# Kernel optimization log

Hardware: AMD Instinct MI355X
Metric: run time of the kernel (lower is better)

The kernel has to match this reference:

```python
import jax, jax.numpy as jnp
import numpy as np

B = 8; N_MELS = 128; T_LEN = 1024; PH = 16; PW = 16
D = 768          # embed_dim
DEPTH = 12
N = 16           # d_state
K = 4            # d_conv (mamba default)
E = 2 * D        # d_inner (expand=2)
R = 48           # dt_rank = ceil(D/16)
NC = 10
LP = (N_MELS // PH) * (T_LEN // PW)   # 512 patch tokens
MID = LP // 2                          # middle cls token position


def layer_norm(x, w, b, eps=1e-5):
    m = x.mean(-1, keepdims=True)
    v = ((x - m) ** 2).mean(-1, keepdims=True)
    return (x - m) * jax.lax.rsqrt(v + eps) * w + b


def dw_conv(x, w, b):
    # x: (B,L,E), w: (E,K) -> causal depthwise conv1d + SiLU (mamba conv branch)
    xt = jnp.transpose(x, (0, 2, 1))
    y = jax.lax.conv_general_dilated(xt, w[:, None, :], (1,), [(K - 1, 0)],
                                     feature_group_count=E,
                                     dimension_numbers=('NCH', 'OIH', 'NCH'))
    return jax.nn.silu(jnp.transpose(y + b[None, :, None], (0, 2, 1)))


def ssm(u, z, xw, dtw, dtb, A_log, Dp):
    # selective scan: u,z (B,L,E); xw (R+2N,E); dtw (E,R); A_log,Dp (E,N)/(E,)
    dbc = jnp.einsum('ble,re->blr', u, xw)
    dt, Bm, Cm = dbc[..., :R], dbc[..., R:R + N], dbc[..., R + N:]
    delta = jax.nn.softplus(jnp.einsum('blr,er->ble', dt, dtw) + dtb)
    A = -jnp.exp(A_log)  # (E,N)

    def step(h, inp):
        d_t, B_t, C_t, u_t = inp  # (B,E),(B,N),(B,N),(B,E)
        h = h * jnp.exp(d_t[:, :, None] * A) + (d_t * u_t)[:, :, None] * B_t[:, None, :]
        return h, jnp.einsum('ben,bn->be', h, C_t)

    h0 = jnp.zeros((u.shape[0], E, N), u.dtype)
    xs = (jnp.transpose(delta, (1, 0, 2)), jnp.transpose(Bm, (1, 0, 2)),
          jnp.transpose(Cm, (1, 0, 2)), jnp.transpose(u, (1, 0, 2)))
    _, ys = jax.lax.scan(step, h0, xs)
    y = jnp.transpose(ys, (1, 0, 2)) + u * Dp
    return y * jax.nn.silu(z)


def setup_inputs() -> dict:
    key = jax.random.key(0)
    kit = iter(jax.random.split(key, 64))
    def nrm(shape, s=0.02):
        return jax.random.normal(next(kit), shape, jnp.float32) * s
    inp = {}
    inp['x'] = jax.random.normal(next(kit), (B, 1, N_MELS, T_LEN), jnp.float32)
    inp['patch_w'] = nrm((D, 1, PH, PW))
    inp['patch_b'] = jnp.zeros((D,), jnp.float32)
    inp['cls_token'] = nrm((1, 1, D))
    inp['norm_w'] = jnp.ones((DEPTH, D), jnp.float32)
    inp['norm_b'] = jnp.zeros((DEPTH, D), jnp.float32)
    inp['in_proj_w'] = nrm((DEPTH, 2 * E, D))
    for s in ('f', 'b'):
        inp['conv_w_' + s] = nrm((DEPTH, E, K), 0.1)
        inp['conv_b_' + s] = jnp.zeros((DEPTH, E), jnp.float32)
        inp['x_proj_w_' + s] = nrm((DEPTH, R + 2 * N, E))
        inp['dt_proj_w_' + s] = nrm((DEPTH, E, R), 0.1)
        dt = jnp.exp(jax.random.uniform(next(kit), (DEPTH, E), jnp.float32)
                     * (np.log(0.1) - np.log(1e-3)) + np.log(1e-3))
        inp['dt_proj_b_' + s] = jnp.log(jnp.expm1(dt))  # inverse softplus init
        inp['A_log_' + s] = jnp.broadcast_to(
            jnp.log(jnp.arange(1, N + 1, dtype=jnp.float32)), (DEPTH, E, N)) + jnp.zeros((DEPTH, E, N), jnp.float32)
        inp['D_' + s] = jnp.ones((DEPTH, E), jnp.float32)
    inp['out_proj_w'] = nrm((DEPTH, D, E))
    inp['fnorm_w'] = jnp.ones((D,), jnp.float32)
    inp['fnorm_b'] = jnp.zeros((D,), jnp.float32)
    inp['head_norm_w'] = jnp.ones((D,), jnp.float32)
    inp['head_norm_b'] = jnp.zeros((D,), jnp.float32)
    inp['head_w'] = nrm((NC, D))
    inp['head_b'] = jnp.zeros((NC,), jnp.float32)
    return inp


def reference(x, patch_w, patch_b, cls_token, norm_w, norm_b, in_proj_w,
              conv_w_f, conv_b_f, conv_w_b, conv_b_b,
              x_proj_w_f, x_proj_w_b, dt_proj_w_f, dt_proj_b_f,
              dt_proj_w_b, dt_proj_b_b, A_log_f, A_log_b, D_f, D_b,
              out_proj_w, fnorm_w, fnorm_b, head_norm_w, head_norm_b,
              head_w, head_b):
    # patch embed (Conv2d, stride = patch)
    t = jax.lax.conv_general_dilated(x, patch_w, (PH, PW), 'VALID',
                                     dimension_numbers=('NCHW', 'OIHW', 'NCHW'))
    t = t + patch_b[None, :, None, None]
    b = t.shape[0]
    tok = jnp.transpose(t.reshape(b, D, -1), (0, 2, 1))  # (B, LP, D)
    cls = jnp.broadcast_to(cls_token, (b, 1, D))
    h = jnp.concatenate([tok[:, :MID], cls, tok[:, MID:]], axis=1)  # middle cls token
    for i in range(DEPTH):
        hn = layer_norm(h, norm_w[i], norm_b[i])
        xz = jnp.einsum('bld,ed->ble', hn, in_proj_w[i])
        xm, z = xz[..., :E], xz[..., E:]
        # forward direction
        xf = dw_conv(xm, conv_w_f[i], conv_b_f[i])
        yf = ssm(xf, z, x_proj_w_f[i], dt_proj_w_f[i], dt_proj_b_f[i], A_log_f[i], D_f[i])
        # backward direction (bimamba v2): scan over flipped sequence
        xr, zr = xm[:, ::-1], z[:, ::-1]
        xb = dw_conv(xr, conv_w_b[i], conv_b_b[i])
        yb = ssm(xb, zr, x_proj_w_b[i], dt_proj_w_b[i], dt_proj_b_b[i], A_log_b[i], D_b[i])[:, ::-1]
        h = h + jnp.einsum('ble,de->bld', yf + yb, out_proj_w[i])
    h = layer_norm(h, fnorm_w, fnorm_b)
    feat = h[:, MID]  # middle cls token feature
    feat = layer_norm(feat, head_norm_w, head_norm_b)
    return jnp.einsum('bd,cd->bc', feat, head_w) + head_b
```

## Files before the change

### kernel.cpp

```cpp
#include <hip/hip_runtime.h>
#include <cstddef>
#include <cstdint>

#define NB     8
#define L_SEQ  513
#define DMODEL 768
#define EDIM   1536
#define XZDIM  3072
#define NSTATE 16
#define DBCW   80
#define RDIM   48
#define ROWS   (NB*L_SEQ)
#define RE     ((size_t)ROWS*EDIM)
#define KSPLIT_DBC 8

typedef unsigned short u16;
typedef __bf16 bf16x8 __attribute__((ext_vector_type(8)));
typedef float  f32x4  __attribute__((ext_vector_type(4)));

__device__ __forceinline__ u16 f2b(float f) {
  uint32_t x = __float_as_uint(f);
  uint32_t r = x + 0x7fffu + ((x >> 16) & 1u);
  return (u16)(r >> 16);
}
__device__ __forceinline__ float b2flo(uint32_t w){ return __uint_as_float(w << 16); }
__device__ __forceinline__ float b2fhi(uint32_t w){ return __uint_as_float(w & 0xffff0000u); }

__device__ __forceinline__ void glds16(const void* g, void* l) {
  __builtin_amdgcn_global_load_lds(
      (const __attribute__((address_space(1))) uint32_t*)g,
      (__attribute__((address_space(3))) uint32_t*)l, 16, 0, 0);
}

__global__ __launch_bounds__(256) void f2b_k(const float* __restrict__ in,
                                             u16* __restrict__ out, int n)
{
  int i = (blockIdx.x*256 + threadIdx.x) * 4;
  if (i >= n) return;
  float4 v = *reinterpret_cast<const float4*>(in + i);
  ushort4 o;
  o.x = f2b(v.x); o.y = f2b(v.y); o.z = f2b(v.z); o.w = f2b(v.w);
  *reinterpret_cast<ushort4*>(out + i) = o;
}

__global__ __launch_bounds__(256) void f2b2_k(const float* __restrict__ a,
                                              const float* __restrict__ b,
                                              u16* __restrict__ oa,
                                              u16* __restrict__ ob,
                                              int n1, int n2)
{
  int i = (blockIdx.x*256 + threadIdx.x) * 4;
  if (i < n1) {
    float4 v = *reinterpret_cast<const float4*>(a + i);
    ushort4 o; o.x=f2b(v.x); o.y=f2b(v.y); o.z=f2b(v.z); o.w=f2b(v.w);
    *reinterpret_cast<ushort4*>(oa + i) = o;
  } else {
    int j = i - n1;
    if (j < n2) {
      float4 v = *reinterpret_cast<const float4*>(b + j);
      ushort4 o; o.x=f2b(v.x); o.y=f2b(v.y); o.z=f2b(v.z); o.w=f2b(v.w);
      int row = j / EDIM, col = j - row*EDIM;
      u16* dst = ob + (size_t)row*XZDIM + col;
      *reinterpret_cast<ushort4*>(dst)        = o;
      *reinterpret_cast<ushort4*>(dst + EDIM) = o;
    }
  }
}

__global__ __launch_bounds__(256) void cvt_dtw_k(const float* __restrict__ in,
                                                 u16* __restrict__ out, int nrows)
{
  int idx = blockIdx.x*256 + threadIdx.x;
  if (idx >= nrows*16) return;
  int row = idx >> 4, c4 = (idx & 15) * 4;
  ushort4 o; o.x = o.y = o.z = o.w = 0;
  if (c4 < RDIM) {
    float4 v = *reinterpret_cast<const float4*>(in + (size_t)row*RDIM + c4);
    o.x = f2b(v.x); o.y = f2b(v.y); o.z = f2b(v.z); o.w = f2b(v.w);
  }
  *reinterpret_cast<ushort4*>(out + (size_t)row*64 + c4) = o;
}

__global__ __launch_bounds__(256) void im2col_k(const float* __restrict__ x,
                                                u16* __restrict__ P)
{
  int idx = blockIdx.x*256 + threadIdx.x;
  int col4 = (idx & 63) * 4;
  int r = idx >> 6;
  int b = r >> 9, p = r & 511;
  int ph = p >> 6, pcol = p & 63;
  int i = col4 >> 4, j = col4 & 15;
  const float* src = x + (size_t)b*131072 + (size_t)(ph*16 + i)*1024 + pcol*16 + j;
  float4 v = *reinterpret_cast<const float4*>(src);
  ushort4 o;
  o.x = f2b(v.x); o.y = f2b(v.y); o.z = f2b(v.z); o.w = f2b(v.w);
  *reinterpret_cast<ushort4*>(P + (size_t)r*256 + col4) = o;
}

__global__ __launch_bounds__(256) void insert_k(const float* __restrict__ tokf,
                                                const float* __restrict__ cls,
                                                float* __restrict__ h)
{
  int idx = blockIdx.x*256 + threadIdx.x;
  if (idx >= ROWS*192) return;
  int d4 = (idx % 192) * 4;
  int row = idx / 192;
  int b = row / L_SEQ, l = row - b*L_SEQ;
  float4 v;
  if (l == 256) v = *reinterpret_cast<const float4*>(cls + d4);
  else {
    int p = (l < 256) ? l : l - 1;
    v = *reinterpret_cast<const float4*>(tokf + ((size_t)(b*512 + p))*DMODEL + d4);
  }
  *reinterpret_cast<float4*>(h + (size_t)row*DMODEL + d4) = v;
}

__device__ __forceinline__ void wave_reduce2(float& s, float& ss) {
  #pragma unroll
  for (int o = 32; o; o >>= 1) { s += __shfl_down(s, o); ss += __shfl_down(ss, o); }
}

__global__ __launch_bounds__(256) void layernorm_k(
    const float* __restrict__ x, const float* __restrict__ w,
    const float* __restrict__ b, u16* __restrict__ y)
{
  int row = blockIdx.x;
  const float* xr = x + (size_t)row*DMODEL;
  u16*         yr = y + (size_t)row*DMODEL;
  int t = threadIdx.x;
  float v0 = xr[t], v1 = xr[t+256], v2 = xr[t+512];
  float s = v0+v1+v2, ss = v0*v0 + v1*v1 + v2*v2;
  wave_reduce2(s, ss);
  __shared__ float sm[8];
  if ((t & 63) == 0) { sm[t>>6] = s; sm[4 + (t>>6)] = ss; }
  __syncthreads();
  s  = sm[0]+sm[1]+sm[2]+sm[3];
  ss = sm[4]+sm[5]+sm[6]+sm[7];
  float mean = s * (1.f/768.f);
  float var  = ss * (1.f/768.f) - mean*mean;
  float rstd = rsqrtf(var + 1e-5f);
  yr[t]     = f2b((v0-mean)*rstd*w[t]     + b[t]);
  yr[t+256] = f2b((v1-mean)*rstd*w[t+256] + b[t+256]);
  yr[t+512] = f2b((v2-mean)*rstd*w[t+512] + b[t+512]);
}

__global__ __launch_bounds__(256) void gemm_bf16_k(
    const u16* __restrict__ A, int lda,
    const u16* __restrict__ W, int ldw,
    float* __restrict__ C, u16* __restrict__ Cb,
    int ldc, int M, int Ncols, int K,
    const float* __restrict__ bias, int epilogue,
    int zsplit, size_t bsA, size_t bsW, size_t bsC, size_t bsBias)
{
  __shared__ __align__(16) u16 Asl[2][4096];
  __shared__ __align__(16) u16 Wsl[2][4096];
  const int tid = threadIdx.x;
  const int bm = blockIdx.y << 7, bn = blockIdx.x << 7;
  const int wv = tid >> 6, ln = tid & 63;
  const int wr = (wv >> 1) << 6, wc = (wv & 1) << 6;

  int kb = 0, ke = K;
  {
    int zb = (int)blockIdx.z;
    int dir = zb / zsplit, kslab = zb - dir*zsplit;
    A += (size_t)dir * bsA;
    W += (size_t)dir * bsW;
    if (C)  C  += (size_t)dir * bsC;
    if (Cb) Cb += (size_t)dir * bsC;
    if (bias) bias += (size_t)dir * bsBias;
    if (zsplit > 1) {
      int ksl = K / zsplit;
      kb = kslab * ksl; ke = kb + ksl;
      C += (size_t)kslab * (size_t)M * (size_t)ldc;
    }
  }

  const int q0 = (ln >> 4) * 8;
  const int r0 = wv*16 + (ln & 15);
  const int r1 = (wv+4)*16 + (ln & 15);

  int ar0 = bm + r0; if (ar0 >= M) ar0 = M-1;
  int ar1 = bm + r1; if (ar1 >= M) ar1 = M-1;
  int nr0 = bn + r0; if (nr0 >= Ncols) nr0 = Ncols-1;
  int nr1 = bn + r1; if (nr1 >= Ncols) nr1 = Ncols-1;
  const u16* A0 = A + (size_t)ar0*lda + q0;
  const u16* A1 = A + (size_t)ar1*lda + q0;
  const u16* W0 = W + (size_t)nr0*ldw + q0;
  const u16* W1 = W + (size_t)nr1*ldw + q0;

  auto STAGE = [&](int buf, int k0) {
    char* ab = (char*)&Asl[buf][0];
    char* wb = (char*)&Wsl[buf][0];
    glds16(A0 + k0, ab + wv*1024);
    glds16(A1 + k0, ab + 4096 + wv*1024);
    glds16(W0 + k0, wb + wv*1024);
    glds16(W1 + k0, wb + 4096 + wv*1024);
  };

  f32x4 acc[4][4];
  #pragma unroll
  for (int m = 0; m < 4; ++m)
    #pragma unroll
    for (int n = 0; n < 4; ++n) acc[m][n] = (f32x4){0.f,0.f,0.f,0.f};

  const int niter = (ke - kb) >> 5;
  STAGE(0, kb);
  for (int it = 0; it < niter; ++it) {
    const int p = it & 1;
    if (it + 1 < niter) {
      STAGE(p ^ 1, kb + (it + 1) * 32);
      asm volatile("s_waitcnt vmcnt(4)" ::: "memory");
    } else {
      asm volatile("s_waitcnt vmcnt(0)" ::: "memory");
    }
    __builtin_amdgcn_s_barrier();
    bf16x8 fa[4], fb[4];
    #pragma unroll
    for (int m = 0; m < 4; ++m)
      fa[m] = *reinterpret_cast<const bf16x8*>(&Asl[p][((wr>>4)+m)*512 + ln*8]);
    #pragma unroll
    for (int n = 0; n < 4; ++n)
      fb[n] = *reinterpret_cast<const bf16x8*>(&Wsl[p][((wc>>4)+n)*512 + ln*8]);
    #pragma unroll
    for (int m = 0; m < 4; ++m)
      #pragma unroll
      for (int n = 0; n < 4; ++n)
        acc[m][n] = __builtin_amdgcn_mfma_f32_16x16x32_bf16(fa[m], fb[n], acc[m][n], 0, 0, 0);
    __builtin_amdgcn_s_barrier();
  }

  const int crow0 = bm + wr + ((ln >> 4) << 2);
  const int ccol0 = bn + wc + (ln & 15);
  #pragma unroll
  for (int m = 0; m < 4; ++m) {
    #pragma unroll
    for (int q = 0; q < 4; ++q) {
      int row = crow0 + m*16 + q;
      if (row >= M) continue;
      #pragma unroll
      for (int n = 0; n < 4; ++n) {
        int col = ccol0 + n*16;
        if (col >= Ncols) continue;
        float v = acc[m][n][q];
        if (epilogue == 0) {
          C[(size_t)row*ldc + col] = v;
        } else if (epilogue == 1) {
          C[(size_t)row*ldc + col] += v;
        } else if (epilogue == 2) {
          v += bias[col];
          v = fmaxf(v, 0.f) + log1pf(__expf(-fabsf(v)));
          Cb[(size_t)row*ldc + col] = f2b(v);
        } else if (epilogue == 3) {
          C[(size_t)row*ldc + col] = v + bias[col];
        } else {
          if (col < EDIM) C[(size_t)row*EDIM + col] = v;
          else            Cb[(size_t)row*EDIM + (col - EDIM)] = f2b(v);
        }
      }
    }
  }
}

__global__ void reduce_split2_k(const float* __restrict__ part,
                                float* __restrict__ dbc2, u16* __restrict__ dt48,
                                int nsplit)
{
  int i = blockIdx.x * 256 + threadIdx.x;
  if (i >= 2*ROWS*DBCW) return;
  int dir = i / (ROWS*DBCW);
  int j   = i - dir*(ROWS*DBCW);
  const float* p = part + (size_t)dir*nsplit*(ROWS*DBCW);
  float s = 0.f;
  for (int z = 0; z < nsplit; ++z) s += p[(size_t)z*(ROWS*DBCW) + j];
  dbc2[i] = s;
  int row = j / DBCW, col = j - row*DBCW;
  if (col < RDIM)    dt48[(size_t)dir*ROWS*64 + (size_t)row*64 + col] = f2b(s);
  else if (col < 64) dt48[(size_t)dir*ROWS*64 + (size_t)row*64 + col] = 0;
}

__global__ __launch_bounds__(256) void dwconv_silu_k(
    const float* __restrict__ xm,
    const float* __restrict__ w_f, const float* __restrict__ w_b,
    const float* __restrict__ b_f, const float* __restrict__ b_b,
    u16* __restrict__ outb2)
{
  const int dir = blockIdx.y;
  const float* w    = dir ? w_b : w_f;
  const float* bias = dir ? b_b : b_f;
  u16* outb = outb2 + (size_t)dir*RE;
  int idx = blockIdx.x * 256 + threadIdx.x;
  int r = idx / (EDIM/4);
  int e4 = (idx - r*(EDIM/4)) * 4;
  int b = r / L_SEQ, t = r - b*L_SEQ;
  float4 acc = *reinterpret_cast<const float4*>(&bias[e4]);
  float4 wq0 = *reinterpret_cast<const float4*>(&w[(size_t)(e4+0)*4]);
  float4 wq1 = *reinterpret_cast<const float4*>(&w[(size_t)(e4+1)*4]);
  float4 wq2 = *reinterpret_cast<const float4*>(&w[(size_t)(e4+2)*4]);
  float4 wq3 = *reinterpret_cast<const float4*>(&w[(size_t)(e4+3)*4]);
  #pragma unroll
  for (int k = 0; k < 4; ++k) {
    int tt = t - 3 + k;
    if (tt >= 0) {
      int phys = dir ? (L_SEQ-1 - tt) : tt;
      float4 xv = *reinterpret_cast<const float4*>(
          &xm[((size_t)b*L_SEQ + phys)*EDIM + e4]);
      float w0 = (k==0)?wq0.x:(k==1)?wq0.y:(k==2)?wq0.z:wq0.w;
      float w1 = (k==0)?wq1.x:(k==1)?wq1.y:(k==2)?wq1.z:wq1.w;
      float w2 = (k==0)?wq2.x:(k==1)?wq2.y:(k==2)?wq2.z:wq2.w;
      float w3 = (k==0)?wq3.x:(k==1)?wq3.y:(k==2)?wq3.z:wq3.w;
      acc.x = fmaf(xv.x, w0, acc.x);
      acc.y = fmaf(xv.y, w1, acc.y);
      acc.z = fmaf(xv.z, w2, acc.z);
      acc.w = fmaf(xv.w, w3, acc.w);
    }
  }
  float4 sv;
  sv.x = acc.x / (1.f + __expf(-acc.x));
  sv.y = acc.y / (1.f + __expf(-acc.y));
  sv.z = acc.z / (1.f + __expf(-acc.z));
  sv.w = acc.w / (1.f + __expf(-acc.w));
  ushort4 ob;
  ob.x = f2b(sv.x); ob.y = f2b(sv.y); ob.z = f2b(sv.z); ob.w = f2b(sv.w);
  *reinterpret_cast<ushort4*>(&outb[(size_t)r*EDIM + e4]) = ob;
}

__device__ __forceinline__ float quad_sum(float v) {
  v += __int_as_float(__builtin_amdgcn_update_dpp(0, __float_as_int(v), 0xB1, 0xf, 0xf, true));
  v += __int_as_float(__builtin_amdgcn_update_dpp(0, __float_as_int(v), 0x4E, 0xf, 0xf, true));
  return v;
}

#define TC 32
#define NCH ((L_SEQ + TC - 1) / TC)

__global__ __launch_bounds__(256) void ssm_scan_k(
    const u16* __restrict__ deltab2, const u16* __restrict__ ub2,
    const float* __restrict__ dbc2,
    const float* __restrict__ Alf, const float* __restrict__ Alb,
    const float* __restrict__ Dpf, const float* __restrict__ Dpb,
    const u16* __restrict__ zb,  u16* __restrict__ yhalf)
{
  __shared__ __align__(16) float dd[2][TC][16];
  __shared__ __align__(16) float us[2][TC][16];
  __shared__ __align__(16) float Bs[2][16][TC+4];
  __shared__ __align__(16) float Cs[2][16][TC+4];
  __shared__ __align__(16) float hc[TC][16][4];

  const int dir = blockIdx.z;
  const u16*   db  = deltab2 + (size_t)dir*RE;
  const u16*   ub  = ub2     + (size_t)dir*RE;
  const float* dbc = dbc2    + (size_t)dir*ROWS*DBCW;
  const float* A_log = dir ? Alb : Alf;
  const float* Dp    = dir ? Dpb : Dpf;

  const int tid = threadIdx.x;
  const int g = tid >> 4, n = tid & 15;
  const int b = blockIdx.y;
  const int e0 = blockIdx.x * 16;
  const size_t rb = (size_t)b * L_SEQ;

  const float a2 = -__expf(A_log[(size_t)(e0+g)*NSTATE + n]) * 1.44269504f;
  const bool wlane = (n & 3) == 0;
  const int  qn = n >> 2;

  const int ss_ = tid >> 3;
  const int c2  = (tid & 7) * 2;
  const int j4  = (tid & 7) * 4;
  const float dp0 = Dp[e0 + c2], dp1 = Dp[e0 + c2 + 1];

  uint32_t dvb = 0, uvb = 0;
  float4 bcv = make_float4(0,0,0,0);

  auto LOAD = [&](int c) {
    int Tn = min(TC, L_SEQ - c*TC);
    if (ss_ < Tn) {
      size_t r = rb + c*TC + ss_;
      dvb = *reinterpret_cast<const uint32_t*>(&db[r*EDIM + e0 + c2]);
      uvb = *reinterpret_cast<const uint32_t*>(&ub[r*EDIM + e0 + c2]);
      bcv = *reinterpret_cast<const float4*>(&dbc[r*DBCW + RDIM + j4]);
    }
  };
  auto STORE = [&](int p, int c) {
    int Tn = min(TC, L_SEQ - c*TC);
    if (ss_ < Tn) {
      dd[p][ss_][c2] = b2flo(dvb); dd[p][ss_][c2+1] = b2fhi(dvb);
      us[p][ss_][c2] = b2flo(uvb); us[p][ss_][c2+1] = b2fhi(uvb);
      if (j4 < 16) {
        Bs[p][j4  ][ss_] = bcv.x; Bs[p][j4+1][ss_] = bcv.y;
        Bs[p][j4+2][ss_] = bcv.z; Bs[p][j4+3][ss_] = bcv.w;
      } else {
        Cs[p][j4-16][ss_] = bcv.x; Cs[p][j4-15][ss_] = bcv.y;
        Cs[p][j4-14][ss_] = bcv.z; Cs[p][j4-13][ss_] = bcv.w;
      }
    }
  };

  float hst = 0.f;
  LOAD(0);
  STORE(0, 0);
  __syncthreads();

  int p = 0;
  for (int c = 0; c < NCH; ++c) {
    const int t0 = c * TC;
    const int T  = min(TC, L_SEQ - t0);
    if (c + 1 < NCH) LOAD(c + 1);

    int s = 0;
    for (; s + 3 < T; s += 4) {
      float4 Bv = *reinterpret_cast<const float4*>(&Bs[p][n][s]);
      float4 Cv = *reinterpret_cast<const float4*>(&Cs[p][n][s]);
      #pragma unroll
      for (int i = 0; i < 4; ++i) {
        float Bt = (i==0)?Bv.x:(i==1)?Bv.y:(i==2)?Bv.z:Bv.w;
        float Ct = (i==0)?Cv.x:(i==1)?Cv.y:(i==2)?Cv.z:Cv.w;
        float d  = dd[p][s+i][g];
        float uu = us[p][s+i][g];
        hst = fmaf(hst, exp2f(d * a2), (d * uu) * Bt);
        float v = quad_sum(hst * Ct);
        if (wlane) hc[s+i][g][qn] = v;
      }
    }
    for (; s < T; ++s) {
      float Bt = Bs[p][n][s], Ct = Cs[p][n][s];
      float d  = dd[p][s][g];
      float uu = us[p][s][g];
      hst = fmaf(hst, exp2f(d * a2), (d * uu) * Bt);
      float v = quad_sum(hst * Ct);
      if (wlane) hc[s][g][qn] = v;
    }
    __syncthreads();

    if (ss_ < T) {
      int t = t0 + ss_;
      int phys = dir ? (L_SEQ-1 - t) : t;
      size_t pr = rb + phys;
      float4 p0 = *reinterpret_cast<const float4*>(&hc[ss_][c2][0]);
      float4 p1 = *reinterpret_cast<const float4*>(&hc[ss_][c2+1][0]);
      float y0 = (p0.x + p0.y) + (p0.z + p0.w);
      float y1 = (p1.x + p1.y) + (p1.z + p1.w);
      y0 = fmaf(us[p][ss_][c2],   dp0, y0);
      y1 = fmaf(us[p][ss_][c2+1], dp1, y1);
      uint32_t zw = *reinterpret_cast<const uint32_t*>(&zb[pr*EDIM + e0 + c2]);
      float z0 = b2flo(zw), z1 = b2fhi(zw);
      y0 *= z0 / (1.f + __expf(-z0));
      y1 *= z1 / (1.f + __expf(-z1));
      ushort2 o; o.x = f2b(y0); o.y = f2b(y1);
      *reinterpret_cast<ushort2*>(&yhalf[((size_t)pr*2 + dir)*EDIM + e0 + c2]) = o;
    }
    if (c + 1 < NCH) STORE(p ^ 1, c + 1);
    __syncthreads();
    p ^= 1;
  }
}

__global__ __launch_bounds__(256) void head_k(
    const float* __restrict__ h,
    const float* __restrict__ fnw, const float* __restrict__ fnb,
    const float* __restrict__ hnw, const float* __restrict__ hnb,
    const float* __restrict__ hw,  const float* __restrict__ hb,
    float* __restrict__ out)
{
  int b = blockIdx.x, t = threadIdx.x;
  const float* xr = h + ((size_t)b*L_SEQ + 256)*DMODEL;
  __shared__ float feat[DMODEL];
  __shared__ float sm[8];
  float v0 = xr[t], v1 = xr[t+256], v2 = xr[t+512];
  float s = v0+v1+v2, ss = v0*v0+v1*v1+v2*v2;
  wave_reduce2(s, ss);
  if ((t & 63) == 0) { sm[t>>6] = s; sm[4+(t>>6)] = ss; }
  __syncthreads();
  s = sm[0]+sm[1]+sm[2]+sm[3]; ss = sm[4]+sm[5]+sm[6]+sm[7];
  float mean = s*(1.f/768.f), var = ss*(1.f/768.f) - mean*mean;
  float rstd = rsqrtf(var + 1e-5f);
  float f0 = (v0-mean)*rstd*fnw[t]     + fnb[t];
  float f1 = (v1-mean)*rstd*fnw[t+256] + fnb[t+256];
  float f2 = (v2-mean)*rstd*fnw[t+512] + fnb[t+512];
  s = f0+f1+f2; ss = f0*f0+f1*f1+f2*f2;
  wave_reduce2(s, ss);
  __syncthreads();
  if ((t & 63) == 0) { sm[t>>6] = s; sm[4+(t>>6)] = ss; }
  __syncthreads();
  s = sm[0]+sm[1]+sm[2]+sm[3]; ss = sm[4]+sm[5]+sm[6]+sm[7];
  mean = s*(1.f/768.f); var = ss*(1.f/768.f) - mean*mean;
  rstd = rsqrtf(var + 1e-5f);
  feat[t]     = (f0-mean)*rstd*hnw[t]     + hnb[t];
  feat[t+256] = (f1-mean)*rstd*hnw[t+256] + hnb[t+256];
  feat[t+512] = (f2-mean)*rstd*hnw[t+512] + hnb[t+512];
  __syncthreads();
  for (int c = 0; c < 10; ++c) {
    float d = 0.f;
    for (int i = t; i < DMODEL; i += 256) d = fmaf(feat[i], hw[(size_t)c*DMODEL + i], d);
    #pragma unroll
    for (int o = 32; o; o >>= 1) d += __shfl_down(d, o);
    __syncthreads();
    if ((t & 63) == 0) sm[t>>6] = d;
    __syncthreads();
    if (t == 0) out[b*10 + c] = sm[0]+sm[1]+sm[2]+sm[3] + hb[c];
  }
}

extern "C" void kernel_launch(void* const* d_in, const int* in_sizes, int n_in,
                              void* d_out, int out_size, void* d_ws, size_t ws_size,
                              hipStream_t stream)
{
  (void)in_sizes; (void)n_in; (void)out_size; (void)ws_size;
  const float* x           = (const float*)d_in[0];
  const float* patch_w     = (const float*)d_in[1];
  const float* patch_b     = (const float*)d_in[2];
  const float* cls_tok     = (const float*)d_in[3];
  const float* norm_w      = (const float*)d_in[4];
  const float* norm_b      = (const float*)d_in[5];
  const float* in_proj_w   = (const float*)d_in[6];
  const float* conv_w_f    = (const float*)d_in[7];
  const float* conv_b_f    = (const float*)d_in[8];
  const float* x_proj_w_f  = (const float*)d_in[9];
  const float* dt_proj_w_f = (const float*)d_in[10];
  const float* dt_proj_b_f = (const float*)d_in[11];
  const float* A_log_f     = (const float*)d_in[12];
  const float* D_f         = (const float*)d_in[13];
  const float* conv_w_b    = (const float*)d_in[14];
  const float* conv_b_b    = (const float*)d_in[15];
  const float* x_proj_w_b  = (const float*)d_in[16];
  const float* dt_proj_w_b = (const float*)d_in[17];
  const float* dt_proj_b_b = (const float*)d_in[18];
  const float* A_log_b     = (const float*)d_in[19];
  const float* D_b         = (const float*)d_in[20];
  const float* out_proj_w  = (const float*)d_in[21];
  const float* fnorm_w     = (const float*)d_in[22];
  const float* fnorm_b     = (const float*)d_in[23];
  const float* head_norm_w = (const float*)d_in[24];
  const float* head_norm_b = (const float*)d_in[25];
  const float* head_w      = (const float*)d_in[26];
  const float* head_b      = (const float*)d_in[27];
  float* out = (float*)d_out;

  float* ws = (float*)d_ws;
  float* h       = ws;        ws += (size_t)ROWS*DMODEL;
  u16*   hn      = (u16*)ws;  ws += (size_t)ROWS*DMODEL/2;
  float* xmf     = ws;        ws += RE;
  u16*   zb16    = (u16*)ws;  ws += RE/2;
  u16*   ubufb2  = (u16*)ws;  ws += RE;
  float* dbc2    = ws;        ws += (size_t)2*ROWS*DBCW;
  u16*   dt48b2  = (u16*)ws;  ws += (size_t)2*ROWS*64/2;
  u16*   deltab2 = (u16*)ws;  ws += RE;
  u16*   yhalf2  = (u16*)ws;  ws += RE;
  u16*   wbf_a   = (u16*)ws;  ws += (size_t)XZDIM*DMODEL/2;
  u16*   wbdup   = (u16*)ws;  ws += (size_t)DMODEL*XZDIM/2;
  u16*   pwbf    = (u16*)ws;  ws += (size_t)DMODEL*256/2;
  u16*   xwbf    = (u16*)ws;  ws += (size_t)2*12*DBCW*EDIM/2;
  u16*   dtwbf   = (u16*)ws;  ws += (size_t)2*12*EDIM*64/2;
  float* dtb2    = ws;        ws += (size_t)2*12*EDIM;
  float* dbcp    = (float*)deltab2;
  u16*   Pim     = ubufb2;
  float* tokf    = (float*)deltab2;

  f2b_k<<<(DMODEL*256)/1024, 256, 0, stream>>>(patch_w, pwbf, DMODEL*256);
  f2b_k<<<(12*DBCW*EDIM)/1024, 256, 0, stream>>>(x_proj_w_f, xwbf, 12*DBCW*EDIM);
  f2b_k<<<(12*DBCW*EDIM)/1024, 256, 0, stream>>>(x_proj_w_b, xwbf + (size_t)12*DBCW*EDIM, 12*DBCW*EDIM);
  cvt_dtw_k<<<(12*EDIM*16)/256, 256, 0, stream>>>(dt_proj_w_f, dtwbf, 12*EDIM);
  cvt_dtw_k<<<(12*EDIM*16)/256, 256, 0, stream>>>(dt_proj_w_b, dtwbf + (size_t)12*EDIM*64, 12*EDIM);
  hipMemcpyAsync(dtb2,           dt_proj_b_f, (size_t)12*EDIM*4, hipMemcpyDeviceToDevice, stream);
  hipMemcpyAsync(dtb2 + 12*EDIM, dt_proj_b_b, (size_t)12*EDIM*4, hipMemcpyDeviceToDevice, stream);

  im2col_k<<<(4096*64)/256, 256, 0, stream>>>(x, Pim);
  {
    dim3 g(DMODEL/128, 4096/128);
    gemm_bf16_k<<<g, 256, 0, stream>>>(Pim, 256, pwbf, 256, tokf, nullptr,
                                       DMODEL, 4096, DMODEL, 256, patch_b, 3,
                                       1, 0, 0, 0, 0);
  }
  insert_k<<<(ROWS*192 + 255)/256, 256, 0, stream>>>(tokf, cls_tok, h);

  const int MT = (ROWS + 127)/128;

  for (int i = 0; i < 12; ++i) {
    f2b2_k<<<(XZDIM*DMODEL + DMODEL*EDIM)/1024, 256, 0, stream>>>(
        in_proj_w + (size_t)i*XZDIM*DMODEL, out_proj_w + (size_t)i*DMODEL*EDIM,
        wbf_a, wbdup, XZDIM*DMODEL, DMODEL*EDIM);
    layernorm_k<<<ROWS, 256, 0, stream>>>(h, norm_w + (size_t)i*DMODEL,
                                          norm_b + (size_t)i*DMODEL, hn);
    {
      dim3 g(XZDIM/128, MT);
      gemm_bf16_k<<<g, 256, 0, stream>>>(hn, DMODEL, wbf_a, DMODEL,
                                         xmf, zb16, EDIM, ROWS, XZDIM, DMODEL,
                                         nullptr, 4, 1, 0, 0, 0, 0);
    }
    {
      dim3 g((ROWS*EDIM/4)/256, 2);
      dwconv_silu_k<<<g, 256, 0, stream>>>(xmf,
          conv_w_f + (size_t)i*EDIM*4, conv_w_b + (size_t)i*EDIM*4,
          conv_b_f + (size_t)i*EDIM,   conv_b_b + (size_t)i*EDIM, ubufb2);
    }
    {
      dim3 g(1, MT, 2*KSPLIT_DBC);
      gemm_bf16_k<<<g, 256, 0, stream>>>(ubufb2, EDIM,
          xwbf + (size_t)i*DBCW*EDIM, EDIM,
          dbcp, nullptr, DBCW, ROWS, DBCW, EDIM, nullptr, 0,
          KSPLIT_DBC, RE, (size_t)12*DBCW*EDIM, (size_t)KSPLIT_DBC*ROWS*DBCW, 0);
      reduce_split2_k<<<(2*ROWS*DBCW + 255)/256, 256, 0, stream>>>(
          dbcp, dbc2, dt48b2, KSPLIT_DBC);
    }
    {
      dim3 g(EDIM/128, MT, 2);
      gemm_bf16_k<<<g, 256, 0, stream>>>(dt48b2, 64,
          dtwbf + (size_t)i*EDIM*64, 64,
          nullptr, deltab2, EDIM, ROWS, EDIM, 64, dtb2 + (size_t)i*EDIM, 2,
          1, (size_t)ROWS*64, (size_t)12*EDIM*64, RE, (size_t)12*EDIM);
    }
    {
      dim3 g(EDIM/16, NB, 2);
      ssm_scan_k<<<g, 256, 0, stream>>>(deltab2, ubufb2, dbc2,
          A_log_f + (size_t)i*EDIM*NSTATE, A_log_b + (size_t)i*EDIM*NSTATE,
          D_f + (size_t)i*EDIM, D_b + (size_t)i*EDIM, zb16, yhalf2);
    }
    {
      dim3 g(DMODEL/128, MT);
      gemm_bf16_k<<<g, 256, 0, stream>>>(yhalf2, XZDIM, wbdup, XZDIM,
                                         h, nullptr, DMODEL, ROWS, DMODEL, XZDIM,
                                         nullptr, 1, 1, 0, 0, 0, 0);
    }
  }

  head_k<<<NB, 256, 0, stream>>>(h, fnorm_w, fnorm_b, head_norm_w, head_norm_b,
                                 head_w, head_b, out);
}
```

Baseline: 5.299 ms.

## Sum bidirectional outputs before out_proj, hoist weight casts, drop split-K dbc GEMM

The forward and backward scan outputs are now written to separate buffers and summed in bf16 by a new add kernel. This halves the K dimension of the out_proj GEMM and removes the duplicated out_proj weight layout. When the workspace is large enough, in_proj and out_proj weights for all 12 layers are cast to bf16 once up front instead of once per layer. The x_proj (dbc) GEMM drops its 8-way split-K and the separate reduce kernel, writing dbc and the padded dt input straight from a new epilogue. In exchange, the dbc GEMM runs with far fewer blocks, and the bf16 pre-sum adds one more rounding step.

```diff
diff --git a/kernel.cpp b/kernel.cpp
--- a/kernel.cpp
+++ b/kernel.cpp
@@ -12,7 +12,6 @@
 #define RDIM   48
 #define ROWS   (NB*L_SEQ)
 #define RE     ((size_t)ROWS*EDIM)
-#define KSPLIT_DBC 8
 
 typedef unsigned short u16;
 typedef __bf16 bf16x8 __attribute__((ext_vector_type(8)));
@@ -59,10 +58,7 @@
     if (j < n2) {
       float4 v = *reinterpret_cast<const float4*>(b + j);
       ushort4 o; o.x=f2b(v.x); o.y=f2b(v.y); o.z=f2b(v.z); o.w=f2b(v.w);
-      int row = j / EDIM, col = j - row*EDIM;
-      u16* dst = ob + (size_t)row*XZDIM + col;
-      *reinterpret_cast<ushort4*>(dst)        = o;
-      *reinterpret_cast<ushort4*>(dst + EDIM) = o;
+      *reinterpret_cast<ushort4*>(ob + j) = o;
     }
   }
 }
@@ -150,7 +146,7 @@
     float* __restrict__ C, u16* __restrict__ Cb,
     int ldc, int M, int Ncols, int K,
     const float* __restrict__ bias, int epilogue,
-    int zsplit, size_t bsA, size_t bsW, size_t bsC, size_t bsBias)
+    int zsplit, size_t bsA, size_t bsW, size_t bsC, size_t bsCb, size_t bsBias)
 {
   __shared__ __align__(16) u16 Asl[2][4096];
   __shared__ __align__(16) u16 Wsl[2][4096];
@@ -166,7 +162,7 @@
     A += (size_t)dir * bsA;
     W += (size_t)dir * bsW;
     if (C)  C  += (size_t)dir * bsC;
-    if (Cb) Cb += (size_t)dir * bsC;
+    if (Cb) Cb += (size_t)dir * bsCb;
     if (bias) bias += (size_t)dir * bsBias;
     if (zsplit > 1) {
       int ksl = K / zsplit;
@@ -252,30 +248,17 @@
           Cb[(size_t)row*ldc + col] = f2b(v);
         } else if (epilogue == 3) {
           C[(size_t)row*ldc + col] = v + bias[col];
-        } else {
+        } else if (epilogue == 4) {
           if (col < EDIM) C[(size_t)row*EDIM + col] = v;
           else            Cb[(size_t)row*EDIM + (col - EDIM)] = f2b(v);
+        } else {
+          C[(size_t)row*ldc + col] = v;
+          if (col < RDIM)    Cb[(size_t)row*64 + col] = f2b(v);
+          else if (col < 64) Cb[(size_t)row*64 + col] = 0;
         }
       }
     }
   }
-}
-
-__global__ void reduce_split2_k(const float* __restrict__ part,
-                                float* __restrict__ dbc2, u16* __restrict__ dt48,
-                                int nsplit)
-{
-  int i = blockIdx.x * 256 + threadIdx.x;
-  if (i >= 2*ROWS*DBCW) return;
-  int dir = i / (ROWS*DBCW);
-  int j   = i - dir*(ROWS*DBCW);
-  const float* p = part + (size_t)dir*nsplit*(ROWS*DBCW);
-  float s = 0.f;
-  for (int z = 0; z < nsplit; ++z) s += p[(size_t)z*(ROWS*DBCW) + j];
-  dbc2[i] = s;
-  int row = j / DBCW, col = j - row*DBCW;
-  if (col < RDIM)    dt48[(size_t)dir*ROWS*64 + (size_t)row*64 + col] = f2b(s);
-  else if (col < 64) dt48[(size_t)dir*ROWS*64 + (size_t)row*64 + col] = 0;
 }
 
 __global__ __launch_bounds__(256) void dwconv_silu_k(
@@ -352,6 +335,7 @@
   const float* dbc = dbc2    + (size_t)dir*ROWS*DBCW;
   const float* A_log = dir ? Alb : Alf;
   const float* Dp    = dir ? Dpb : Dpf;
+  u16* yh = yhalf + (size_t)dir*RE;
 
   const int tid = threadIdx.x;
   const int g = tid >> 4, n = tid & 15;
@@ -446,12 +430,31 @@
       y0 *= z0 / (1.f + __expf(-z0));
       y1 *= z1 / (1.f + __expf(-z1));
       ushort2 o; o.x = f2b(y0); o.y = f2b(y1);
-      *reinterpret_cast<ushort2*>(&yhalf[((size_t)pr*2 + dir)*EDIM + e0 + c2]) = o;
+      *reinterpret_cast<ushort2*>(&yh[pr*EDIM + e0 + c2]) = o;
     }
     if (c + 1 < NCH) STORE(p ^ 1, c + 1);
     __syncthreads();
     p ^= 1;
   }
+}
+
+__global__ __launch_bounds__(256) void add_ybf_k(const u16* __restrict__ yhalf,
+                                                 u16* __restrict__ ybf)
+{
+  size_t i = ((size_t)blockIdx.x*256 + threadIdx.x) * 8;
+  uint4 a = *reinterpret_cast<const uint4*>(yhalf + i);
+  uint4 b = *reinterpret_cast<const uint4*>(yhalf + RE + i);
+  uint32_t av[4] = {a.x, a.y, a.z, a.w};
+  uint32_t bv[4] = {b.x, b.y, b.z, b.w};
+  uint32_t ov[4];
+  #pragma unroll
+  for (int q = 0; q < 4; ++q) {
+    float lo = b2flo(av[q]) + b2flo(bv[q]);
+    float hi = b2fhi(av[q]) + b2fhi(bv[q]);
+    ov[q] = (uint32_t)f2b(lo) | ((uint32_t)f2b(hi) << 16);
+  }
+  uint4 o = {ov[0], ov[1], ov[2], ov[3]};
+  *reinterpret_cast<uint4*>(ybf + i) = o;
 }
 
 __global__ __launch_bounds__(256) void head_k(
@@ -504,7 +507,7 @@
                               void* d_out, int out_size, void* d_ws, size_t ws_size,
                               hipStream_t stream)
 {
-  (void)in_sizes; (void)n_in; (void)out_size; (void)ws_size;
+  (void)in_sizes; (void)n_in; (void)out_size;
   const float* x           = (const float*)d_in[0];
   const float* patch_w     = (const float*)d_in[1];
   const float* patch_b     = (const float*)d_in[2];
@@ -537,23 +540,27 @@
 
   float* ws = (float*)d_ws;
   float* h       = ws;        ws += (size_t)ROWS*DMODEL;
-  u16*   hn      = (u16*)ws;  ws += (size_t)ROWS*DMODEL/2;
+  u16*   hn      = (u16*)ws;  ws += RE/2;
+  u16*   ybf     = hn;
   float* xmf     = ws;        ws += RE;
   u16*   zb16    = (u16*)ws;  ws += RE/2;
   u16*   ubufb2  = (u16*)ws;  ws += RE;
   float* dbc2    = ws;        ws += (size_t)2*ROWS*DBCW;
   u16*   dt48b2  = (u16*)ws;  ws += (size_t)2*ROWS*64/2;
   u16*   deltab2 = (u16*)ws;  ws += RE;
-  u16*   yhalf2  = (u16*)ws;  ws += RE;
+  u16*   yhalf   = (u16*)ws;  ws += RE;
   u16*   wbf_a   = (u16*)ws;  ws += (size_t)XZDIM*DMODEL/2;
-  u16*   wbdup   = (u16*)ws;  ws += (size_t)DMODEL*XZDIM/2;
+  u16*   wbf_b   = (u16*)ws;  ws += (size_t)DMODEL*EDIM/2;
   u16*   pwbf    = (u16*)ws;  ws += (size_t)DMODEL*256/2;
   u16*   xwbf    = (u16*)ws;  ws += (size_t)2*12*DBCW*EDIM/2;
   u16*   dtwbf   = (u16*)ws;  ws += (size_t)2*12*EDIM*64/2;
   float* dtb2    = ws;        ws += (size_t)2*12*EDIM;
-  float* dbcp    = (float*)deltab2;
-  u16*   Pim     = ubufb2;
-  float* tokf    = (float*)deltab2;
+  u16*   wfull_a = (u16*)ws;
+  u16*   wfull_b = wfull_a + (size_t)12*XZDIM*DMODEL;
+  size_t need_full = (size_t)((char*)(wfull_b + (size_t)12*DMODEL*EDIM) - (char*)d_ws);
+  const bool full = ws_size >= need_full;
+  u16*   Pim  = ubufb2;
+  float* tokf = (float*)deltab2;
 
   f2b_k<<<(DMODEL*256)/1024, 256, 0, stream>>>(patch_w, pwbf, DMODEL*256);
   f2b_k<<<(12*DBCW*EDIM)/1024, 256, 0, stream>>>(x_proj_w_f, xwbf, 12*DBCW*EDIM);
@@ -562,29 +569,37 @@
   cvt_dtw_k<<<(12*EDIM*16)/256, 256, 0, stream>>>(dt_proj_w_b, dtwbf + (size_t)12*EDIM*64, 12*EDIM);
   hipMemcpyAsync(dtb2,           dt_proj_b_f, (size_t)12*EDIM*4, hipMemcpyDeviceToDevice, stream);
   hipMemcpyAsync(dtb2 + 12*EDIM, dt_proj_b_b, (size_t)12*EDIM*4, hipMemcpyDeviceToDevice, stream);
+  if (full) {
+    f2b_k<<<(12*XZDIM*DMODEL)/1024, 256, 0, stream>>>(in_proj_w,  wfull_a, 12*XZDIM*DMODEL);
+    f2b_k<<<(12*DMODEL*EDIM)/1024,  256, 0, stream>>>(out_proj_w, wfull_b, 12*DMODEL*EDIM);
+  }
 
   im2col_k<<<(4096*64)/256, 256, 0, stream>>>(x, Pim);
   {
     dim3 g(DMODEL/128, 4096/128);
     gemm_bf16_k<<<g, 256, 0, stream>>>(Pim, 256, pwbf, 256, tokf, nullptr,
                                        DMODEL, 4096, DMODEL, 256, patch_b, 3,
-                                       1, 0, 0, 0, 0);
+                                       1, 0, 0, 0, 0, 0);
   }
   insert_k<<<(ROWS*192 + 255)/256, 256, 0, stream>>>(tokf, cls_tok, h);
 
   const int MT = (ROWS + 127)/128;
 
   for (int i = 0; i < 12; ++i) {
-    f2b2_k<<<(XZDIM*DMODEL + DMODEL*EDIM)/1024, 256, 0, stream>>>(
-        in_proj_w + (size_t)i*XZDIM*DMODEL, out_proj_w + (size_t)i*DMODEL*EDIM,
-        wbf_a, wbdup, XZDIM*DMODEL, DMODEL*EDIM);
+    const u16* wA = full ? (wfull_a + (size_t)i*XZDIM*DMODEL) : wbf_a;
+    const u16* wB = full ? (wfull_b + (size_t)i*DMODEL*EDIM)  : wbf_b;
+    if (!full) {
+      f2b2_k<<<(XZDIM*DMODEL + DMODEL*EDIM)/1024, 256, 0, stream>>>(
+          in_proj_w + (size_t)i*XZDIM*DMODEL, out_proj_w + (size_t)i*DMODEL*EDIM,
+          wbf_a, wbf_b, XZDIM*DMODEL, DMODEL*EDIM);
+    }
     layernorm_k<<<ROWS, 256, 0, stream>>>(h, norm_w + (size_t)i*DMODEL,
                                           norm_b + (size_t)i*DMODEL, hn);
     {
       dim3 g(XZDIM/128, MT);
-      gemm_bf16_k<<<g, 256, 0, stream>>>(hn, DMODEL, wbf_a, DMODEL,
+      gemm_bf16_k<<<g, 256, 0, stream>>>(hn, DMODEL, wA, DMODEL,
                                          xmf, zb16, EDIM, ROWS, XZDIM, DMODEL,
-                                         nullptr, 4, 1, 0, 0, 0, 0);
+                                         nullptr, 4, 1, 0, 0, 0, 0, 0);
     }
     {
       dim3 g((ROWS*EDIM/4)/256, 2);
@@ -593,32 +608,31 @@
           conv_b_f + (size_t)i*EDIM,   conv_b_b + (size_t)i*EDIM, ubufb2);
     }
     {
-      dim3 g(1, MT, 2*KSPLIT_DBC);
+      dim3 g(1, MT, 2);
       gemm_bf16_k<<<g, 256, 0, stream>>>(ubufb2, EDIM,
           xwbf + (size_t)i*DBCW*EDIM, EDIM,
-          dbcp, nullptr, DBCW, ROWS, DBCW, EDIM, nullptr, 0,
-          KSPLIT_DBC, RE, (size_t)12*DBCW*EDIM, (size_t)KSPLIT_DBC*ROWS*DBCW, 0);
-      reduce_split2_k<<<(2*ROWS*DBCW + 255)/256, 256, 0, stream>>>(
-          dbcp, dbc2, dt48b2, KSPLIT_DBC);
+          dbc2, dt48b2, DBCW, ROWS, DBCW, EDIM, nullptr, 5,
+          1, RE, (size_t)12*DBCW*EDIM, (size_t)ROWS*DBCW, (size_t)ROWS*64, 0);
     }
     {
       dim3 g(EDIM/128, MT, 2);
       gemm_bf16_k<<<g, 256, 0, stream>>>(dt48b2, 64,
           dtwbf + (size_t)i*EDIM*64, 64,
           nullptr, deltab2, EDIM, ROWS, EDIM, 64, dtb2 + (size_t)i*EDIM, 2,
-          1, (size_t)ROWS*64, (size_t)12*EDIM*64, RE, (size_t)12*EDIM);
+          1, (size_t)ROWS*64, (size_t)12*EDIM*64, 0, RE, (size_t)12*EDIM);
     }
     {
       dim3 g(EDIM/16, NB, 2);
       ssm_scan_k<<<g, 256, 0, stream>>>(deltab2, ubufb2, dbc2,
           A_log_f + (size_t)i*EDIM*NSTATE, A_log_b + (size_t)i*EDIM*NSTATE,
-          D_f + (size_t)i*EDIM, D_b + (size_t)i*EDIM, zb16, yhalf2);
-    }
+          D_f + (size_t)i*EDIM, D_b + (size_t)i*EDIM, zb16, yhalf);
+    }
+    add_ybf_k<<<(int)(RE/8/256), 256, 0, stream>>>(yhalf, ybf);
     {
       dim3 g(DMODEL/128, MT);
-      gemm_bf16_k<<<g, 256, 0, stream>>>(yhalf2, XZDIM, wbdup, XZDIM,
-                                         h, nullptr, DMODEL, ROWS, DMODEL, XZDIM,
-                                         nullptr, 1, 1, 0, 0, 0, 0);
+      gemm_bf16_k<<<g, 256, 0, stream>>>(ybf, EDIM, wB, EDIM,
+                                         h, nullptr, DMODEL, ROWS, DMODEL, EDIM,
+                                         nullptr, 1, 1, 0, 0, 0, 0, 0);
     }
   }
 
```

Result: faster. 5.136 ms (-3.1%).
